# Performance work log

Measured on AMD Instinct MI355X. Metric: run time of the kernel, lower is better.

The kernel has to match this reference:

```python
import jax, jax.numpy as jnp
import numpy as np

B, T, IN, H, OUT = 512, 1024, 16, 128, 1


def _lstm_layer(x_tbd, W_ih, W_hh, b_ih, b_hh):
    """Single LSTM layer, PyTorch gate order (i, f, g, o).
    x_tbd: [T, B, D_in] -> returns [T, B, H]."""
    Tn, Bn = x_tbd.shape[0], x_tbd.shape[1]
    # Precompute input contribution for all timesteps: [T, B, 4H]
    gx = jnp.einsum('tbd,gd->tbg', x_tbd, W_ih) + b_ih + b_hh
    h0 = jnp.zeros((Bn, H), x_tbd.dtype)
    c0 = jnp.zeros((Bn, H), x_tbd.dtype)

    def step(carry, gx_t):
        h, c = carry
        gates = gx_t + h @ W_hh.T  # [B, 4H]
        i = jax.nn.sigmoid(gates[:, 0 * H:1 * H])
        f = jax.nn.sigmoid(gates[:, 1 * H:2 * H])
        g = jnp.tanh(gates[:, 2 * H:3 * H])
        o = jax.nn.sigmoid(gates[:, 3 * H:4 * H])
        c = f * c + i * g
        h = o * jnp.tanh(c)
        return (h, c), h

    _, hs = jax.lax.scan(step, (h0, c0), gx)
    return hs  # [T, B, H]


def setup_inputs() -> dict:
    key = jax.random.key(0)
    ks = jax.random.split(key, 12)
    s = 1.0 / np.sqrt(H)  # PyTorch LSTM init scale
    return {
        'x': jax.random.normal(ks[0], (B, T, IN), jnp.float32),
        'W_ih0': jax.random.uniform(ks[1], (4 * H, IN), jnp.float32, -s, s),
        'W_hh0': jax.random.uniform(ks[2], (4 * H, H), jnp.float32, -s, s),
        'b_ih0': jax.random.uniform(ks[3], (4 * H,), jnp.float32, -s, s),
        'b_hh0': jax.random.uniform(ks[4], (4 * H,), jnp.float32, -s, s),
        'W_ih1': jax.random.uniform(ks[5], (4 * H, H), jnp.float32, -s, s),
        'W_hh1': jax.random.uniform(ks[6], (4 * H, H), jnp.float32, -s, s),
        'b_ih1': jax.random.uniform(ks[7], (4 * H,), jnp.float32, -s, s),
        'b_hh1': jax.random.uniform(ks[8], (4 * H,), jnp.float32, -s, s),
        'W_fc': jax.random.uniform(ks[9], (OUT, H), jnp.float32, -s, s),
        'b_fc': jax.random.uniform(ks[10], (OUT,), jnp.float32, -s, s),
    }


def reference(x, W_ih0, W_hh0, b_ih0, b_hh0, W_ih1, W_hh1, b_ih1, b_hh1, W_fc, b_fc):
    x_tbd = jnp.transpose(x, (1, 0, 2))  # [T, B, IN]
    h1 = _lstm_layer(x_tbd, W_ih0, W_hh0, b_ih0, b_hh0)  # [T, B, H]
    h2 = _lstm_layer(h1, W_ih1, W_hh1, b_ih1, b_hh1)     # [T, B, H]
    out = jnp.transpose(h2, (1, 0, 2))  # [B, T, H]
    out = jax.nn.relu(out)
    out = out @ W_fc.T + b_fc  # [B, T, 1]
    out = jax.nn.relu(out)
    return out
```

## Files before the change

kernel.cpp:

```cpp
#include <hip/hip_runtime.h>

#define T_SEQ  1024
#define NBATCH 512
#define IN_DIM 16
#define HDIM   128
#define G4     (4 * HDIM)
#define TC     64
#define NCHUNK (T_SEQ / TC)
#define NWGH   128

typedef unsigned short ushort_t;
typedef __attribute__((ext_vector_type(8))) _Float16 f16x8;
typedef __attribute__((ext_vector_type(4))) float f32x4;

#define MFMA16(a, b, c) __builtin_amdgcn_mfma_f32_16x16x32_f16((a), (b), (c), 0, 0, 0)

__device__ __forceinline__ float sigf(float x) {
  return __builtin_amdgcn_rcpf(1.0f + __expf(-x));
}
__device__ __forceinline__ float tanhf_fast(float x) {
  return 1.0f - 2.0f * __builtin_amdgcn_rcpf(1.0f + __expf(2.0f * x));
}
__device__ __forceinline__ ushort_t f16_bits(float f) {
  const _Float16 h = (_Float16)f;
  return __builtin_bit_cast(unsigned short, h);
}
__device__ __forceinline__ void split_f16(float f, ushort_t* hi, ushort_t* lo) {
  const _Float16 h = (_Float16)f;
  *hi = __builtin_bit_cast(unsigned short, h);
  const _Float16 l = (_Float16)(f - (float)h);
  *lo = __builtin_bit_cast(unsigned short, l);
}
__device__ __forceinline__ void bar_lds() {
  asm volatile("s_waitcnt lgkmcnt(0)\n\ts_barrier" ::: "memory");
}

__global__ __launch_bounds__(256) void prep_weights(
    const float* __restrict__ Whh0, const float* __restrict__ Whh1,
    const float* __restrict__ Wih0, const float* __restrict__ Wih1,
    ushort_t* __restrict__ w0h, ushort_t* __restrict__ w0l,
    ushort_t* __restrict__ w1h, ushort_t* __restrict__ w1l,
    ushort_t* __restrict__ wxh, ushort_t* __restrict__ wxl,
    ushort_t* __restrict__ wi1h, ushort_t* __restrict__ wi1l)
{
  const int idx = blockIdx.x * 256 + threadIdx.x;
  if (idx < 512 * HDIM) {
    split_f16(Whh0[idx], &w0h[idx], &w0l[idx]);
    split_f16(Whh1[idx], &w1h[idx], &w1l[idx]);
    split_f16(Wih1[idx], &wi1h[idx], &wi1l[idx]);
  }
  if (idx < 512 * 32) {
    const int g = idx >> 5, k = idx & 31;
    const float f = (k < IN_DIM) ? Wih0[g * IN_DIM + k] : 0.0f;
    split_f16(f, &wxh[idx], &wxl[idx]);
  }
}

struct L0LDS {
  __align__(16) ushort_t hfA[4][144];
  __align__(16) ushort_t hfB[4][144];
  __align__(16) ushort_t xlds[4][TC][32];
  __align__(16) float gx0s[8 * 4 * 128 * 4];
};
struct L1LDS {
  __align__(16) ushort_t hfA[4][144];
  __align__(16) ushort_t hfB[4][144];
  __align__(16) ushort_t h2l[TC][4][136];
  __align__(16) float wfl[HDIM];
};

__global__ __launch_bounds__(512, 2) void lstm_pipe(
    const float* __restrict__ x,
    const ushort_t* __restrict__ w0h,
    const ushort_t* __restrict__ wxh, const ushort_t* __restrict__ wxl,
    const float* __restrict__ bih0, const float* __restrict__ bhh0,
    const ushort_t* __restrict__ wi1h,
    const ushort_t* __restrict__ w1h,
    const float* __restrict__ bih1, const float* __restrict__ bhh1,
    const float* __restrict__ Wfc, const float* __restrict__ bfc,
    float* __restrict__ out,
    float* __restrict__ h1s, float* __restrict__ c1s,
    float* __restrict__ h2s, float* __restrict__ c2s,
    ushort_t* __restrict__ h1buf,
    float* __restrict__ gx1buf,
    int ch)
{
  const int tid  = threadIdx.x;
  const int lane = tid & 63;
  const int wv   = tid >> 6;
  const int row  = lane & 15;
  const int kq   = lane >> 4;
  const int bq   = row >> 2;
  const int j    = wv * 16 + row;

  constexpr size_t POOL =
      sizeof(L0LDS) > sizeof(L1LDS) ? sizeof(L0LDS) : sizeof(L1LDS);
  __shared__ __align__(16) char pool[POOL];

  if (blockIdx.x < NWGH) {
    if (ch >= NCHUNK) return;
    L0LDS& S = *(L0LDS*)pool;
    const int w  = blockIdx.x;
    const int b0 = w * 4;

    f16x8 Bh[4][4], Bxh[4], Bxl[4];
#pragma unroll
    for (int i = 0; i < 4; ++i) {
      const int g = i * 128 + j;
#pragma unroll
      for (int kt = 0; kt < 4; ++kt)
        Bh[i][kt] = *(const f16x8*)&w0h[g * HDIM + kt * 32 + kq * 8];
      Bxh[i] = *(const f16x8*)&wxh[g * 32 + kq * 8];
      Bxl[i] = *(const f16x8*)&wxl[g * 32 + kq * 8];
    }

    {
      const int r = tid >> 1, half = tid & 1;
      const int b = r >> 6, ts = r & (TC - 1);
      const float* src =
          &x[((size_t)(b0 + b) * T_SEQ + ch * TC + ts) * IN_DIM + half * 8];
      const float4 v0 = *(const float4*)&src[0];
      const float4 v1 = *(const float4*)&src[4];
      ushort_t* dst = &S.xlds[b][ts][half * 8];
      dst[0] = f16_bits(v0.x); dst[1] = f16_bits(v0.y);
      dst[2] = f16_bits(v0.z); dst[3] = f16_bits(v0.w);
      dst[4] = f16_bits(v1.x); dst[5] = f16_bits(v1.y);
      dst[6] = f16_bits(v1.z); dst[7] = f16_bits(v1.w);
      *(float4*)&S.xlds[b][ts][16 + half * 8] = (float4){0.f, 0.f, 0.f, 0.f};
    }

    float bz[4];
#pragma unroll
    for (int i = 0; i < 4; ++i) bz[i] = bih0[i * 128 + j] + bhh0[i * 128 + j];
    float hc = h1s[(size_t)(b0 + kq) * HDIM + j];
    float cc = c1s[(size_t)(b0 + kq) * HDIM + j];
    S.hfA[kq][j] = f16_bits(hc);
    __syncthreads();

    ushort_t* hbp = h1buf + ((size_t)(ch & 1) * NWGH + w) * (TC * 4 * HDIM) +
                    (size_t)kq * HDIM + j;

#define L0_STEP(HIN, HOUT, TT)                                              \
  {                                                                         \
    const float4 zcu =                                                      \
        *(const float4*)&S.gx0s[((((TT) & 7) * 4 + kq) * 128 + j) * 4];     \
    f32x4 aH[4];                                                            \
    _Pragma("unroll") for (int i = 0; i < 4; ++i)                           \
        aH[i] = (f32x4){0.f, 0.f, 0.f, 0.f};                                \
    _Pragma("unroll") for (int kt = 0; kt < 4; ++kt) {                      \
      const f16x8 ah = *(const f16x8*)&S.HIN[bq][kt * 32 + kq * 8];         \
      _Pragma("unroll") for (int i = 0; i < 4; ++i)                         \
          aH[i] = MFMA16(ah, Bh[i][kt], aH[i]);                             \
    }                                                                       \
    const float ig = sigf(aH[0][0] + zcu.x);                                \
    const float fg = sigf(aH[1][0] + zcu.y);                                \
    const float gg = tanhf_fast(aH[2][0] + zcu.z);                          \
    const float og = sigf(aH[3][0] + zcu.w);                                \
    cc = fg * cc + ig * gg;                                                 \
    hc = og * tanhf_fast(cc);                                               \
    const ushort_t hbits = f16_bits(hc);                                    \
    S.HOUT[kq][j] = hbits;                                                  \
    *hbp = hbits;                                                           \
    hbp += 4 * HDIM;                                                        \
    bar_lds();                                                              \
  }

    for (int sc = 0; sc < TC / 8; ++sc) {
#pragma unroll
      for (int mt = 0; mt < 2; ++mt) {
        const f16x8 a =
            *(const f16x8*)&S.xlds[row & 3][sc * 8 + mt * 4 + (row >> 2)][kq * 8];
        f32x4 acc[4];
#pragma unroll
        for (int i = 0; i < 4; ++i) acc[i] = (f32x4){0.f, 0.f, 0.f, 0.f};
#pragma unroll
        for (int i = 0; i < 4; ++i) acc[i] = MFMA16(a, Bxh[i], acc[i]);
#pragma unroll
        for (int i = 0; i < 4; ++i) acc[i] = MFMA16(a, Bxl[i], acc[i]);
#pragma unroll
        for (int r = 0; r < 4; ++r) {
          float4 o;
          o.x = acc[0][r] + bz[0];
          o.y = acc[1][r] + bz[1];
          o.z = acc[2][r] + bz[2];
          o.w = acc[3][r] + bz[3];
          *(float4*)&S.gx0s[(((mt * 4 + kq) * 4 + r) * 128 + j) * 4] = o;
        }
      }
      bar_lds();
#pragma unroll 1
      for (int q = 0; q < 4; ++q) {
        const int tt = sc * 8 + q * 2;
        L0_STEP(hfA, hfB, tt);
        L0_STEP(hfB, hfA, tt + 1);
      }
    }
#undef L0_STEP

    h1s[(size_t)(b0 + kq) * HDIM + j] = hc;
    c1s[(size_t)(b0 + kq) * HDIM + j] = cc;
  } else {
    if (ch == 0) return;
    L1LDS& S = *(L1LDS*)pool;
    const int w  = blockIdx.x - NWGH;
    const int b0 = w * 4;

    const ushort_t* hb =
        h1buf + ((size_t)((ch - 1) & 1) * NWGH + w) * (TC * 4 * HDIM);
    float* gx = gx1buf + (size_t)w * (TC * 4 * HDIM * 4);

    if (tid < HDIM) S.wfl[tid] = Wfc[tid];

    {
      f16x8 Gh[4][4];
      float bz1[4];
#pragma unroll
      for (int i = 0; i < 4; ++i) {
        const int g = i * 128 + j;
#pragma unroll
        for (int kt = 0; kt < 4; ++kt)
          Gh[i][kt] = *(const f16x8*)&wi1h[g * HDIM + kt * 32 + kq * 8];
        bz1[i] = bih1[i * 128 + j] + bhh1[i * 128 + j];
      }
#pragma unroll 2
      for (int mt = 0; mt < TC * 4 / 16; ++mt) {
        f32x4 acc[4];
#pragma unroll
        for (int i = 0; i < 4; ++i) acc[i] = (f32x4){0.f, 0.f, 0.f, 0.f};
#pragma unroll
        for (int kt = 0; kt < 4; ++kt) {
          const f16x8 a =
              *(const f16x8*)&hb[(size_t)(mt * 16 + row) * HDIM + kt * 32 + kq * 8];
#pragma unroll
          for (int i = 0; i < 4; ++i) acc[i] = MFMA16(a, Gh[i][kt], acc[i]);
        }
#pragma unroll
        for (int r = 0; r < 4; ++r) {
          const int m = mt * 16 + kq * 4 + r;
          float4 o;
          o.x = acc[0][r] + bz1[0];
          o.y = acc[1][r] + bz1[1];
          o.z = acc[2][r] + bz1[2];
          o.w = acc[3][r] + bz1[3];
          *(float4*)&gx[((size_t)m * HDIM + j) * 4] = o;
        }
      }
    }

    float hc = h2s[(size_t)(b0 + kq) * HDIM + j];
    float cc = c2s[(size_t)(b0 + kq) * HDIM + j];
    S.hfA[kq][j] = f16_bits(hc);
    __syncthreads();

    f16x8 Rh[4][4];
#pragma unroll
    for (int i = 0; i < 4; ++i) {
      const int g = i * 128 + j;
#pragma unroll
      for (int kt = 0; kt < 4; ++kt)
        Rh[i][kt] = *(const f16x8*)&w1h[g * HDIM + kt * 32 + kq * 8];
    }

    const float4* gxp = (const float4*)&gx[((size_t)kq * HDIM + j) * 4];
    float4 zcc = *gxp;
    gxp += 512;

#define L1_STEP(HIN, HOUT, TT)                                              \
  {                                                                         \
    const float4 zcu = zcc;                                                 \
    if ((TT) + 1 < TC) { zcc = *gxp; gxp += 512; }                          \
    f32x4 aH[4];                                                            \
    _Pragma("unroll") for (int i = 0; i < 4; ++i)                           \
        aH[i] = (f32x4){0.f, 0.f, 0.f, 0.f};                                \
    _Pragma("unroll") for (int kt = 0; kt < 4; ++kt) {                      \
      const f16x8 ah = *(const f16x8*)&S.HIN[bq][kt * 32 + kq * 8];         \
      _Pragma("unroll") for (int i = 0; i < 4; ++i)                         \
          aH[i] = MFMA16(ah, Rh[i][kt], aH[i]);                             \
    }                                                                       \
    const float ig = sigf(aH[0][0] + zcu.x);                                \
    const float fg = sigf(aH[1][0] + zcu.y);                                \
    const float gg = tanhf_fast(aH[2][0] + zcu.z);                          \
    const float og = sigf(aH[3][0] + zcu.w);                                \
    cc = fg * cc + ig * gg;                                                 \
    hc = og * tanhf_fast(cc);                                               \
    const ushort_t hbits = f16_bits(hc);                                    \
    S.HOUT[kq][j] = hbits;                                                  \
    S.h2l[TT][kq][j] = hbits;                                               \
    bar_lds();                                                              \
  }

    for (int tt = 0; tt < TC; tt += 2) {
      L1_STEP(hfA, hfB, tt);
      L1_STEP(hfB, hfA, tt + 1);
    }
#undef L1_STEP

    h2s[(size_t)(b0 + kq) * HDIM + j] = hc;
    c2s[(size_t)(b0 + kq) * HDIM + j] = cc;

    if (tid < TC * 4) {
      const int tt = tid >> 2, b = tid & 3;
      const float bfcv = bfc[0];
      float s0 = 0.f, s1 = 0.f, s2 = 0.f, s3 = 0.f;
#pragma unroll
      for (int q = 0; q < HDIM / 8; ++q) {
        const f16x8 hv = *(const f16x8*)&S.h2l[tt][b][q * 8];
        const float* wq = &S.wfl[q * 8];
        s0 += fmaxf((float)hv[0], 0.f) * wq[0];
        s1 += fmaxf((float)hv[1], 0.f) * wq[1];
        s2 += fmaxf((float)hv[2], 0.f) * wq[2];
        s3 += fmaxf((float)hv[3], 0.f) * wq[3];
        s0 += fmaxf((float)hv[4], 0.f) * wq[4];
        s1 += fmaxf((float)hv[5], 0.f) * wq[5];
        s2 += fmaxf((float)hv[6], 0.f) * wq[6];
        s3 += fmaxf((float)hv[7], 0.f) * wq[7];
      }
      const float s = s0 + s1 + s2 + s3 + bfcv;
      out[(size_t)(b0 + b) * T_SEQ + (ch - 1) * TC + tt] = fmaxf(s, 0.0f);
    }
  }
}

extern "C" void kernel_launch(void* const* d_in, const int* in_sizes, int n_in,
                              void* d_out, int out_size, void* d_ws, size_t ws_size,
                              hipStream_t stream)
{
  const float* x    = (const float*)d_in[0];
  const float* Wih0 = (const float*)d_in[1];
  const float* Whh0 = (const float*)d_in[2];
  const float* bih0 = (const float*)d_in[3];
  const float* bhh0 = (const float*)d_in[4];
  const float* Wih1 = (const float*)d_in[5];
  const float* Whh1 = (const float*)d_in[6];
  const float* bih1 = (const float*)d_in[7];
  const float* bhh1 = (const float*)d_in[8];
  const float* Wfc  = (const float*)d_in[9];
  const float* bfc  = (const float*)d_in[10];
  float* out = (float*)d_out;

  const size_t stateN = (size_t)NBATCH * HDIM;
  float* h1s = (float*)d_ws;
  float* c1s = h1s + stateN;
  float* h2s = c1s + stateN;
  float* c2s = h2s + stateN;
  ushort_t* w0h  = (ushort_t*)(c2s + stateN);
  ushort_t* w0l  = w0h  + stateN;
  ushort_t* w1h  = w0l  + stateN;
  ushort_t* w1l  = w1h  + stateN;
  ushort_t* wi1h = w1l  + stateN;
  ushort_t* wi1l = wi1h + stateN;
  ushort_t* wxh  = wi1l + stateN;
  ushort_t* wxl  = wxh  + 512 * 32;
  ushort_t* h1buf = wxl + 512 * 32;
  float* gx1buf = (float*)(h1buf + (size_t)2 * NWGH * TC * 4 * HDIM);

  (void)hipMemsetAsync(d_ws, 0, 4 * stateN * sizeof(float), stream);
  hipLaunchKernelGGL(prep_weights, dim3(256), dim3(256), 0, stream,
                     Whh0, Whh1, Wih0, Wih1,
                     w0h, w0l, w1h, w1l, wxh, wxl, wi1h, wi1l);

  for (int ch = 0; ch <= NCHUNK; ++ch) {
    hipLaunchKernelGGL(lstm_pipe, dim3(2 * NWGH), dim3(512), 0, stream,
                       x, w0h, wxh, wxl, bih0, bhh0,
                       wi1h, w1h, bih1, bhh1, Wfc, bfc,
                       out, h1s, c1s, h2s, c2s, h1buf, gx1buf, ch);
  }
}
```

Baseline: 926.7 us.

## Co-schedule both LSTM layers in one 1024-thread workgroup with lockstep barriers

Instead of separate workgroups for layer 0 and layer 1, each 1024-thread block runs layer 0 in its first 512 threads and layer 1 in the second 512. Inactive halves execute matching dummy barrier loops so both halves step in lockstep. Layer 1's input projection is moved from a single upfront pass into per-8-step sub-chunks, and the input-weight fragments are reloaded inside the loop to reduce live registers. This halves the grid and co-locates the layers on one CU. In exchange, each layer now waits on the other's step latency, and the 1024-thread bound limits VGPRs per thread, which may cause spills.

```diff
diff --git a/kernel.cpp b/kernel.cpp
--- a/kernel.cpp
+++ b/kernel.cpp
@@ -69,7 +69,7 @@
   __align__(16) float wfl[HDIM];
 };
 
-__global__ __launch_bounds__(512, 2) void lstm_pipe(
+__global__ __launch_bounds__(1024) void lstm_pipe(
     const float* __restrict__ x,
     const ushort_t* __restrict__ w0h,
     const ushort_t* __restrict__ wxh, const ushort_t* __restrict__ wxl,
@@ -86,47 +86,51 @@
     int ch)
 {
   const int tid  = threadIdx.x;
+  const int ltid = tid & 511;
   const int lane = tid & 63;
-  const int wv   = tid >> 6;
+  const int wv   = (tid >> 6) & 7;
   const int row  = lane & 15;
   const int kq   = lane >> 4;
   const int bq   = row >> 2;
   const int j    = wv * 16 + row;
-
-  constexpr size_t POOL =
-      sizeof(L0LDS) > sizeof(L1LDS) ? sizeof(L0LDS) : sizeof(L1LDS);
-  __shared__ __align__(16) char pool[POOL];
-
-  if (blockIdx.x < NWGH) {
-    if (ch >= NCHUNK) return;
-    L0LDS& S = *(L0LDS*)pool;
-    const int w  = blockIdx.x;
-    const int b0 = w * 4;
-
-    f16x8 Bh[4][4], Bxh[4], Bxl[4];
+  const int w    = blockIdx.x;
+  const int b0   = w * 4;
+
+  __shared__ L0LDS S0;
+  __shared__ L1LDS S1;
+
+  if (tid < 512) {
+    if (ch >= NCHUNK) {
+      __syncthreads();
+      for (int sc = 0; sc < TC / 8; ++sc) {
+        __syncthreads();
+        for (int q = 0; q < 8; ++q) bar_lds();
+      }
+      return;
+    }
+
+    f16x8 Bh[4][4];
 #pragma unroll
     for (int i = 0; i < 4; ++i) {
       const int g = i * 128 + j;
 #pragma unroll
       for (int kt = 0; kt < 4; ++kt)
         Bh[i][kt] = *(const f16x8*)&w0h[g * HDIM + kt * 32 + kq * 8];
-      Bxh[i] = *(const f16x8*)&wxh[g * 32 + kq * 8];
-      Bxl[i] = *(const f16x8*)&wxl[g * 32 + kq * 8];
     }
 
     {
-      const int r = tid >> 1, half = tid & 1;
+      const int r = ltid >> 1, half = ltid & 1;
       const int b = r >> 6, ts = r & (TC - 1);
       const float* src =
           &x[((size_t)(b0 + b) * T_SEQ + ch * TC + ts) * IN_DIM + half * 8];
       const float4 v0 = *(const float4*)&src[0];
       const float4 v1 = *(const float4*)&src[4];
-      ushort_t* dst = &S.xlds[b][ts][half * 8];
+      ushort_t* dst = &S0.xlds[b][ts][half * 8];
       dst[0] = f16_bits(v0.x); dst[1] = f16_bits(v0.y);
       dst[2] = f16_bits(v0.z); dst[3] = f16_bits(v0.w);
       dst[4] = f16_bits(v1.x); dst[5] = f16_bits(v1.y);
       dst[6] = f16_bits(v1.z); dst[7] = f16_bits(v1.w);
-      *(float4*)&S.xlds[b][ts][16 + half * 8] = (float4){0.f, 0.f, 0.f, 0.f};
+      *(float4*)&S0.xlds[b][ts][16 + half * 8] = (float4){0.f, 0.f, 0.f, 0.f};
     }
 
     float bz[4];
@@ -134,7 +138,7 @@
     for (int i = 0; i < 4; ++i) bz[i] = bih0[i * 128 + j] + bhh0[i * 128 + j];
     float hc = h1s[(size_t)(b0 + kq) * HDIM + j];
     float cc = c1s[(size_t)(b0 + kq) * HDIM + j];
-    S.hfA[kq][j] = f16_bits(hc);
+    S0.hfA[kq][j] = f16_bits(hc);
     __syncthreads();
 
     ushort_t* hbp = h1buf + ((size_t)(ch & 1) * NWGH + w) * (TC * 4 * HDIM) +
@@ -143,12 +147,12 @@
 #define L0_STEP(HIN, HOUT, TT)                                              \
   {                                                                         \
     const float4 zcu =                                                      \
-        *(const float4*)&S.gx0s[((((TT) & 7) * 4 + kq) * 128 + j) * 4];     \
+        *(const float4*)&S0.gx0s[((((TT) & 7) * 4 + kq) * 128 + j) * 4];    \
     f32x4 aH[4];                                                            \
     _Pragma("unroll") for (int i = 0; i < 4; ++i)                           \
         aH[i] = (f32x4){0.f, 0.f, 0.f, 0.f};                                \
     _Pragma("unroll") for (int kt = 0; kt < 4; ++kt) {                      \
-      const f16x8 ah = *(const f16x8*)&S.HIN[bq][kt * 32 + kq * 8];         \
+      const f16x8 ah = *(const f16x8*)&S0.HIN[bq][kt * 32 + kq * 8];        \
       _Pragma("unroll") for (int i = 0; i < 4; ++i)                         \
           aH[i] = MFMA16(ah, Bh[i][kt], aH[i]);                             \
     }                                                                       \
@@ -159,35 +163,44 @@
     cc = fg * cc + ig * gg;                                                 \
     hc = og * tanhf_fast(cc);                                               \
     const ushort_t hbits = f16_bits(hc);                                    \
-    S.HOUT[kq][j] = hbits;                                                  \
+    S0.HOUT[kq][j] = hbits;                                                 \
     *hbp = hbits;                                                           \
     hbp += 4 * HDIM;                                                        \
     bar_lds();                                                              \
   }
 
     for (int sc = 0; sc < TC / 8; ++sc) {
-#pragma unroll
-      for (int mt = 0; mt < 2; ++mt) {
-        const f16x8 a =
-            *(const f16x8*)&S.xlds[row & 3][sc * 8 + mt * 4 + (row >> 2)][kq * 8];
-        f32x4 acc[4];
-#pragma unroll
-        for (int i = 0; i < 4; ++i) acc[i] = (f32x4){0.f, 0.f, 0.f, 0.f};
-#pragma unroll
-        for (int i = 0; i < 4; ++i) acc[i] = MFMA16(a, Bxh[i], acc[i]);
-#pragma unroll
-        for (int i = 0; i < 4; ++i) acc[i] = MFMA16(a, Bxl[i], acc[i]);
-#pragma unroll
-        for (int r = 0; r < 4; ++r) {
-          float4 o;
-          o.x = acc[0][r] + bz[0];
-          o.y = acc[1][r] + bz[1];
-          o.z = acc[2][r] + bz[2];
-          o.w = acc[3][r] + bz[3];
-          *(float4*)&S.gx0s[(((mt * 4 + kq) * 4 + r) * 128 + j) * 4] = o;
+      {
+        f16x8 Bxh[4], Bxl[4];
+#pragma unroll
+        for (int i = 0; i < 4; ++i) {
+          const int g = i * 128 + j;
+          Bxh[i] = *(const f16x8*)&wxh[g * 32 + kq * 8];
+          Bxl[i] = *(const f16x8*)&wxl[g * 32 + kq * 8];
         }
-      }
-      bar_lds();
+#pragma unroll
+        for (int mt = 0; mt < 2; ++mt) {
+          const f16x8 a = *(const f16x8*)
+              &S0.xlds[row & 3][sc * 8 + mt * 4 + (row >> 2)][kq * 8];
+          f32x4 acc[4];
+#pragma unroll
+          for (int i = 0; i < 4; ++i) acc[i] = (f32x4){0.f, 0.f, 0.f, 0.f};
+#pragma unroll
+          for (int i = 0; i < 4; ++i) acc[i] = MFMA16(a, Bxh[i], acc[i]);
+#pragma unroll
+          for (int i = 0; i < 4; ++i) acc[i] = MFMA16(a, Bxl[i], acc[i]);
+#pragma unroll
+          for (int r = 0; r < 4; ++r) {
+            float4 o;
+            o.x = acc[0][r] + bz[0];
+            o.y = acc[1][r] + bz[1];
+            o.z = acc[2][r] + bz[2];
+            o.w = acc[3][r] + bz[3];
+            *(float4*)&S0.gx0s[(((mt * 4 + kq) * 4 + r) * 128 + j) * 4] = o;
+          }
+        }
+      }
+      __syncthreads();
 #pragma unroll 1
       for (int q = 0; q < 4; ++q) {
         const int tt = sc * 8 + q * 2;
@@ -200,112 +213,125 @@
     h1s[(size_t)(b0 + kq) * HDIM + j] = hc;
     c1s[(size_t)(b0 + kq) * HDIM + j] = cc;
   } else {
-    if (ch == 0) return;
-    L1LDS& S = *(L1LDS*)pool;
-    const int w  = blockIdx.x - NWGH;
-    const int b0 = w * 4;
+    if (ch == 0) {
+      __syncthreads();
+      for (int sc = 0; sc < TC / 8; ++sc) {
+        __syncthreads();
+        for (int q = 0; q < 8; ++q) bar_lds();
+      }
+      return;
+    }
 
     const ushort_t* hb =
         h1buf + ((size_t)((ch - 1) & 1) * NWGH + w) * (TC * 4 * HDIM);
     float* gx = gx1buf + (size_t)w * (TC * 4 * HDIM * 4);
 
-    if (tid < HDIM) S.wfl[tid] = Wfc[tid];
-
-    {
-      f16x8 Gh[4][4];
-      float bz1[4];
-#pragma unroll
-      for (int i = 0; i < 4; ++i) {
-        const int g = i * 128 + j;
-#pragma unroll
-        for (int kt = 0; kt < 4; ++kt)
-          Gh[i][kt] = *(const f16x8*)&wi1h[g * HDIM + kt * 32 + kq * 8];
-        bz1[i] = bih1[i * 128 + j] + bhh1[i * 128 + j];
-      }
-#pragma unroll 2
-      for (int mt = 0; mt < TC * 4 / 16; ++mt) {
-        f32x4 acc[4];
-#pragma unroll
-        for (int i = 0; i < 4; ++i) acc[i] = (f32x4){0.f, 0.f, 0.f, 0.f};
-#pragma unroll
-        for (int kt = 0; kt < 4; ++kt) {
-          const f16x8 a =
-              *(const f16x8*)&hb[(size_t)(mt * 16 + row) * HDIM + kt * 32 + kq * 8];
-#pragma unroll
-          for (int i = 0; i < 4; ++i) acc[i] = MFMA16(a, Gh[i][kt], acc[i]);
-        }
-#pragma unroll
-        for (int r = 0; r < 4; ++r) {
-          const int m = mt * 16 + kq * 4 + r;
-          float4 o;
-          o.x = acc[0][r] + bz1[0];
-          o.y = acc[1][r] + bz1[1];
-          o.z = acc[2][r] + bz1[2];
-          o.w = acc[3][r] + bz1[3];
-          *(float4*)&gx[((size_t)m * HDIM + j) * 4] = o;
-        }
-      }
+    if (ltid < HDIM) S1.wfl[ltid] = Wfc[ltid];
+
+    float bz1[4];
+#pragma unroll
+    for (int i = 0; i < 4; ++i) bz1[i] = bih1[i * 128 + j] + bhh1[i * 128 + j];
+    f16x8 Rh[4][4];
+#pragma unroll
+    for (int i = 0; i < 4; ++i) {
+      const int g = i * 128 + j;
+#pragma unroll
+      for (int kt = 0; kt < 4; ++kt)
+        Rh[i][kt] = *(const f16x8*)&w1h[g * HDIM + kt * 32 + kq * 8];
     }
 
     float hc = h2s[(size_t)(b0 + kq) * HDIM + j];
     float cc = c2s[(size_t)(b0 + kq) * HDIM + j];
-    S.hfA[kq][j] = f16_bits(hc);
+    S1.hfA[kq][j] = f16_bits(hc);
     __syncthreads();
 
-    f16x8 Rh[4][4];
-#pragma unroll
-    for (int i = 0; i < 4; ++i) {
-      const int g = i * 128 + j;
-#pragma unroll
-      for (int kt = 0; kt < 4; ++kt)
-        Rh[i][kt] = *(const f16x8*)&w1h[g * HDIM + kt * 32 + kq * 8];
-    }
-
-    const float4* gxp = (const float4*)&gx[((size_t)kq * HDIM + j) * 4];
-    float4 zcc = *gxp;
-    gxp += 512;
-
-#define L1_STEP(HIN, HOUT, TT)                                              \
+#define L1_STEP(HIN, HOUT, TT, ZCU)                                         \
   {                                                                         \
-    const float4 zcu = zcc;                                                 \
-    if ((TT) + 1 < TC) { zcc = *gxp; gxp += 512; }                          \
     f32x4 aH[4];                                                            \
     _Pragma("unroll") for (int i = 0; i < 4; ++i)                           \
         aH[i] = (f32x4){0.f, 0.f, 0.f, 0.f};                                \
     _Pragma("unroll") for (int kt = 0; kt < 4; ++kt) {                      \
-      const f16x8 ah = *(const f16x8*)&S.HIN[bq][kt * 32 + kq * 8];         \
+      const f16x8 ah = *(const f16x8*)&S1.HIN[bq][kt * 32 + kq * 8];        \
       _Pragma("unroll") for (int i = 0; i < 4; ++i)                         \
           aH[i] = MFMA16(ah, Rh[i][kt], aH[i]);                             \
     }                                                                       \
-    const float ig = sigf(aH[0][0] + zcu.x);                                \
-    const float fg = sigf(aH[1][0] + zcu.y);                                \
-    const float gg = tanhf_fast(aH[2][0] + zcu.z);                          \
-    const float og = sigf(aH[3][0] + zcu.w);                                \
+    const float ig = sigf(aH[0][0] + (ZCU).x);                              \
+    const float fg = sigf(aH[1][0] + (ZCU).y);                              \
+    const float gg = tanhf_fast(aH[2][0] + (ZCU).z);                        \
+    const float og = sigf(aH[3][0] + (ZCU).w);                              \
     cc = fg * cc + ig * gg;                                                 \
     hc = og * tanhf_fast(cc);                                               \
     const ushort_t hbits = f16_bits(hc);                                    \
-    S.HOUT[kq][j] = hbits;                                                  \
-    S.h2l[TT][kq][j] = hbits;                                               \
+    S1.HOUT[kq][j] = hbits;                                                 \
+    S1.h2l[TT][kq][j] = hbits;                                              \
     bar_lds();                                                              \
   }
 
-    for (int tt = 0; tt < TC; tt += 2) {
-      L1_STEP(hfA, hfB, tt);
-      L1_STEP(hfB, hfA, tt + 1);
+    for (int sc = 0; sc < TC / 8; ++sc) {
+      {
+        f16x8 Gh[4][4];
+#pragma unroll
+        for (int i = 0; i < 4; ++i) {
+          const int g = i * 128 + j;
+#pragma unroll
+          for (int kt = 0; kt < 4; ++kt)
+            Gh[i][kt] = *(const f16x8*)&wi1h[g * HDIM + kt * 32 + kq * 8];
+        }
+#pragma unroll
+        for (int mt2 = 0; mt2 < 2; ++mt2) {
+          const int m0 = sc * 32 + mt2 * 16;
+          f32x4 acc[4];
+#pragma unroll
+          for (int i = 0; i < 4; ++i) acc[i] = (f32x4){0.f, 0.f, 0.f, 0.f};
+#pragma unroll
+          for (int kt = 0; kt < 4; ++kt) {
+            const f16x8 a =
+                *(const f16x8*)&hb[(size_t)(m0 + row) * HDIM + kt * 32 + kq * 8];
+#pragma unroll
+            for (int i = 0; i < 4; ++i) acc[i] = MFMA16(a, Gh[i][kt], acc[i]);
+          }
+#pragma unroll
+          for (int r = 0; r < 4; ++r) {
+            const int m = m0 + kq * 4 + r;
+            float4 o;
+            o.x = acc[0][r] + bz1[0];
+            o.y = acc[1][r] + bz1[1];
+            o.z = acc[2][r] + bz1[2];
+            o.w = acc[3][r] + bz1[3];
+            *(float4*)&gx[((size_t)m * HDIM + j) * 4] = o;
+          }
+        }
+      }
+      __syncthreads();
+
+      const float4* gxp =
+          (const float4*)gx + ((size_t)(sc * 8 * 4 + kq) * HDIM + j);
+      float4 zcc = *gxp;
+      gxp += 512;
+#pragma unroll 1
+      for (int q = 0; q < 4; ++q) {
+        const int tt = sc * 8 + q * 2;
+        float4 z0 = zcc;
+        zcc = *gxp; gxp += 512;
+        L1_STEP(hfA, hfB, tt, z0);
+        float4 z1 = zcc;
+        if (q < 3) { zcc = *gxp; gxp += 512; }
+        L1_STEP(hfB, hfA, tt + 1, z1);
+      }
     }
 #undef L1_STEP
 
     h2s[(size_t)(b0 + kq) * HDIM + j] = hc;
     c2s[(size_t)(b0 + kq) * HDIM + j] = cc;
 
-    if (tid < TC * 4) {
-      const int tt = tid >> 2, b = tid & 3;
+    if (ltid < TC * 4) {
+      const int tt = ltid >> 2, b = ltid & 3;
       const float bfcv = bfc[0];
       float s0 = 0.f, s1 = 0.f, s2 = 0.f, s3 = 0.f;
 #pragma unroll
       for (int q = 0; q < HDIM / 8; ++q) {
-        const f16x8 hv = *(const f16x8*)&S.h2l[tt][b][q * 8];
-        const float* wq = &S.wfl[q * 8];
+        const f16x8 hv = *(const f16x8*)&S1.h2l[tt][b][q * 8];
+        const float* wq = &S1.wfl[q * 8];
         s0 += fmaxf((float)hv[0], 0.f) * wq[0];
         s1 += fmaxf((float)hv[1], 0.f) * wq[1];
         s2 += fmaxf((float)hv[2], 0.f) * wq[2];
@@ -360,7 +386,7 @@
                      w0h, w0l, w1h, w1l, wxh, wxl, wi1h, wi1l);
 
   for (int ch = 0; ch <= NCHUNK; ++ch) {
-    hipLaunchKernelGGL(lstm_pipe, dim3(2 * NWGH), dim3(512), 0, stream,
+    hipLaunchKernelGGL(lstm_pipe, dim3(NWGH), dim3(1024), 0, stream,
                        x, w0h, wxh, wxl, bih0, bhh0,
                        wi1h, w1h, bih1, bhh1, Wfc, bfc,
                        out, h1s, c1s, h2s, c2s, h1buf, gx1buf, ch);
```

New measurement: 2.273 ms. 145% more time.

## Process eight batch rows per workgroup and interleave layer-1 input projection per subchunk

Applied to the files above, without the earlier changes.

Halves the number of workgroups per layer and gives each one 8 batch rows, so every recurrent step issues two independent MFMA chains that share the same register-resident weights. This is meant to hide the latency of the serial recurrence chain. Layer 1 now computes its input-gate projection in 4-step subchunks interleaved with the recurrence rather than all upfront, keeps both weight sets resident in registers, and writes h2 to a global buffer instead of LDS for the final FC. The trade-off is more register pressure, fewer active CUs, and an extra global round trip for the FC stage.

```diff
diff --git a/kernel.cpp b/kernel.cpp
--- a/kernel.cpp
+++ b/kernel.cpp
@@ -7,7 +7,7 @@
 #define G4     (4 * HDIM)
 #define TC     64
 #define NCHUNK (T_SEQ / TC)
-#define NWGH   128
+#define NWGH   64
 
 typedef unsigned short ushort_t;
 typedef __attribute__((ext_vector_type(8))) _Float16 f16x8;
@@ -57,15 +57,14 @@
 }
 
 struct L0LDS {
-  __align__(16) ushort_t hfA[4][144];
-  __align__(16) ushort_t hfB[4][144];
-  __align__(16) ushort_t xlds[4][TC][32];
-  __align__(16) float gx0s[8 * 4 * 128 * 4];
+  __align__(16) ushort_t hfA[8][144];
+  __align__(16) ushort_t hfB[8][144];
+  __align__(16) ushort_t xlds[8][TC][32];
+  __align__(16) float gx0s[4 * 8 * 128 * 4];
 };
 struct L1LDS {
-  __align__(16) ushort_t hfA[4][144];
-  __align__(16) ushort_t hfB[4][144];
-  __align__(16) ushort_t h2l[TC][4][136];
+  __align__(16) ushort_t hfA[8][144];
+  __align__(16) ushort_t hfB[8][144];
   __align__(16) float wfl[HDIM];
 };
 
@@ -82,6 +81,7 @@
     float* __restrict__ h1s, float* __restrict__ c1s,
     float* __restrict__ h2s, float* __restrict__ c2s,
     ushort_t* __restrict__ h1buf,
+    ushort_t* __restrict__ h2buf,
     float* __restrict__ gx1buf,
     int ch)
 {
@@ -93,15 +93,13 @@
   const int bq   = row >> 2;
   const int j    = wv * 16 + row;
 
-  constexpr size_t POOL =
-      sizeof(L0LDS) > sizeof(L1LDS) ? sizeof(L0LDS) : sizeof(L1LDS);
-  __shared__ __align__(16) char pool[POOL];
+  __shared__ L0LDS S0;
+  __shared__ L1LDS S1;
 
   if (blockIdx.x < NWGH) {
     if (ch >= NCHUNK) return;
-    L0LDS& S = *(L0LDS*)pool;
     const int w  = blockIdx.x;
-    const int b0 = w * 4;
+    const int b0 = w * 8;
 
     f16x8 Bh[4][4], Bxh[4], Bxl[4];
 #pragma unroll
@@ -114,62 +112,88 @@
       Bxl[i] = *(const f16x8*)&wxl[g * 32 + kq * 8];
     }
 
-    {
-      const int r = tid >> 1, half = tid & 1;
-      const int b = r >> 6, ts = r & (TC - 1);
+#pragma unroll
+    for (int q = 0; q < 2; ++q) {
+      const int idx  = q * 512 + tid;
+      const int half = idx & 1;
+      const int ts   = (idx >> 1) & (TC - 1);
+      const int b    = idx >> 7;
       const float* src =
           &x[((size_t)(b0 + b) * T_SEQ + ch * TC + ts) * IN_DIM + half * 8];
       const float4 v0 = *(const float4*)&src[0];
       const float4 v1 = *(const float4*)&src[4];
-      ushort_t* dst = &S.xlds[b][ts][half * 8];
+      ushort_t* dst = &S0.xlds[b][ts][half * 8];
       dst[0] = f16_bits(v0.x); dst[1] = f16_bits(v0.y);
       dst[2] = f16_bits(v0.z); dst[3] = f16_bits(v0.w);
       dst[4] = f16_bits(v1.x); dst[5] = f16_bits(v1.y);
       dst[6] = f16_bits(v1.z); dst[7] = f16_bits(v1.w);
-      *(float4*)&S.xlds[b][ts][16 + half * 8] = (float4){0.f, 0.f, 0.f, 0.f};
+      *(float4*)&S0.xlds[b][ts][16 + half * 8] = (float4){0.f, 0.f, 0.f, 0.f};
     }
 
     float bz[4];
 #pragma unroll
     for (int i = 0; i < 4; ++i) bz[i] = bih0[i * 128 + j] + bhh0[i * 128 + j];
-    float hc = h1s[(size_t)(b0 + kq) * HDIM + j];
-    float cc = c1s[(size_t)(b0 + kq) * HDIM + j];
-    S.hfA[kq][j] = f16_bits(hc);
+    float hc0 = h1s[(size_t)(b0 + kq) * HDIM + j];
+    float cc0 = c1s[(size_t)(b0 + kq) * HDIM + j];
+    float hc1 = h1s[(size_t)(b0 + 4 + kq) * HDIM + j];
+    float cc1 = c1s[(size_t)(b0 + 4 + kq) * HDIM + j];
+    S0.hfA[kq][j]     = f16_bits(hc0);
+    S0.hfA[4 + kq][j] = f16_bits(hc1);
     __syncthreads();
 
-    ushort_t* hbp = h1buf + ((size_t)(ch & 1) * NWGH + w) * (TC * 4 * HDIM) +
+    ushort_t* hbp = h1buf + ((size_t)(ch & 1) * NWGH + w) * (TC * 8 * HDIM) +
                     (size_t)kq * HDIM + j;
 
 #define L0_STEP(HIN, HOUT, TT)                                              \
   {                                                                         \
-    const float4 zcu =                                                      \
-        *(const float4*)&S.gx0s[((((TT) & 7) * 4 + kq) * 128 + j) * 4];     \
-    f32x4 aH[4];                                                            \
-    _Pragma("unroll") for (int i = 0; i < 4; ++i)                           \
-        aH[i] = (f32x4){0.f, 0.f, 0.f, 0.f};                                \
+    const float4 z0 =                                                       \
+        *(const float4*)&S0.gx0s[((((TT) & 3) * 8 + kq) * 128 + j) * 4];    \
+    const float4 z1 =                                                       \
+        *(const float4*)&S0.gx0s[((((TT) & 3) * 8 + 4 + kq) * 128 + j) * 4];\
+    f32x4 a0[4], a1[4];                                                     \
+    _Pragma("unroll") for (int i = 0; i < 4; ++i) {                         \
+      a0[i] = (f32x4){0.f, 0.f, 0.f, 0.f};                                  \
+      a1[i] = (f32x4){0.f, 0.f, 0.f, 0.f};                                  \
+    }                                                                       \
     _Pragma("unroll") for (int kt = 0; kt < 4; ++kt) {                      \
-      const f16x8 ah = *(const f16x8*)&S.HIN[bq][kt * 32 + kq * 8];         \
+      const f16x8 ah0 = *(const f16x8*)&S0.HIN[bq][kt * 32 + kq * 8];       \
+      const f16x8 ah1 = *(const f16x8*)&S0.HIN[4 + bq][kt * 32 + kq * 8];   \
       _Pragma("unroll") for (int i = 0; i < 4; ++i)                         \
-          aH[i] = MFMA16(ah, Bh[i][kt], aH[i]);                             \
-    }                                                                       \
-    const float ig = sigf(aH[0][0] + zcu.x);                                \
-    const float fg = sigf(aH[1][0] + zcu.y);                                \
-    const float gg = tanhf_fast(aH[2][0] + zcu.z);                          \
-    const float og = sigf(aH[3][0] + zcu.w);                                \
-    cc = fg * cc + ig * gg;                                                 \
-    hc = og * tanhf_fast(cc);                                               \
-    const ushort_t hbits = f16_bits(hc);                                    \
-    S.HOUT[kq][j] = hbits;                                                  \
-    *hbp = hbits;                                                           \
-    hbp += 4 * HDIM;                                                        \
+          a0[i] = MFMA16(ah0, Bh[i][kt], a0[i]);                            \
+      _Pragma("unroll") for (int i = 0; i < 4; ++i)                         \
+          a1[i] = MFMA16(ah1, Bh[i][kt], a1[i]);                            \
+    }                                                                       \
+    {                                                                       \
+      const float ig = sigf(a0[0][0] + z0.x);                               \
+      const float fg = sigf(a0[1][0] + z0.y);                               \
+      const float gg = tanhf_fast(a0[2][0] + z0.z);                         \
+      const float og = sigf(a0[3][0] + z0.w);                               \
+      cc0 = fg * cc0 + ig * gg;                                             \
+      hc0 = og * tanhf_fast(cc0);                                           \
+      const ushort_t hb0 = f16_bits(hc0);                                   \
+      S0.HOUT[kq][j] = hb0;                                                 \
+      hbp[0] = hb0;                                                         \
+    }                                                                       \
+    {                                                                       \
+      const float ig = sigf(a1[0][0] + z1.x);                               \
+      const float fg = sigf(a1[1][0] + z1.y);                               \
+      const float gg = tanhf_fast(a1[2][0] + z1.z);                         \
+      const float og = sigf(a1[3][0] + z1.w);                               \
+      cc1 = fg * cc1 + ig * gg;                                             \
+      hc1 = og * tanhf_fast(cc1);                                           \
+      const ushort_t hb1 = f16_bits(hc1);                                   \
+      S0.HOUT[4 + kq][j] = hb1;                                             \
+      hbp[4 * HDIM] = hb1;                                                  \
+    }                                                                       \
+    hbp += 8 * HDIM;                                                        \
     bar_lds();                                                              \
   }
 
-    for (int sc = 0; sc < TC / 8; ++sc) {
-#pragma unroll
-      for (int mt = 0; mt < 2; ++mt) {
-        const f16x8 a =
-            *(const f16x8*)&S.xlds[row & 3][sc * 8 + mt * 4 + (row >> 2)][kq * 8];
+    for (int sc = 0; sc < TC / 4; ++sc) {
+#pragma unroll
+      for (int g = 0; g < 2; ++g) {
+        const f16x8 a = *(const f16x8*)
+            &S0.xlds[g * 4 + (row & 3)][sc * 4 + (row >> 2)][kq * 8];
         f32x4 acc[4];
 #pragma unroll
         for (int i = 0; i < 4; ++i) acc[i] = (f32x4){0.f, 0.f, 0.f, 0.f};
@@ -184,128 +208,169 @@
           o.y = acc[1][r] + bz[1];
           o.z = acc[2][r] + bz[2];
           o.w = acc[3][r] + bz[3];
-          *(float4*)&S.gx0s[(((mt * 4 + kq) * 4 + r) * 128 + j) * 4] = o;
+          *(float4*)&S0.gx0s[((kq * 8 + g * 4 + r) * 128 + j) * 4] = o;
         }
       }
       bar_lds();
-#pragma unroll 1
-      for (int q = 0; q < 4; ++q) {
-        const int tt = sc * 8 + q * 2;
-        L0_STEP(hfA, hfB, tt);
-        L0_STEP(hfB, hfA, tt + 1);
-      }
+      const int t0s = sc * 4;
+      L0_STEP(hfA, hfB, t0s);
+      L0_STEP(hfB, hfA, t0s + 1);
+      L0_STEP(hfA, hfB, t0s + 2);
+      L0_STEP(hfB, hfA, t0s + 3);
     }
 #undef L0_STEP
 
-    h1s[(size_t)(b0 + kq) * HDIM + j] = hc;
-    c1s[(size_t)(b0 + kq) * HDIM + j] = cc;
+    h1s[(size_t)(b0 + kq) * HDIM + j]     = hc0;
+    c1s[(size_t)(b0 + kq) * HDIM + j]     = cc0;
+    h1s[(size_t)(b0 + 4 + kq) * HDIM + j] = hc1;
+    c1s[(size_t)(b0 + 4 + kq) * HDIM + j] = cc1;
   } else {
     if (ch == 0) return;
-    L1LDS& S = *(L1LDS*)pool;
     const int w  = blockIdx.x - NWGH;
-    const int b0 = w * 4;
+    const int b0 = w * 8;
 
     const ushort_t* hb =
-        h1buf + ((size_t)((ch - 1) & 1) * NWGH + w) * (TC * 4 * HDIM);
-    float* gx = gx1buf + (size_t)w * (TC * 4 * HDIM * 4);
-
-    if (tid < HDIM) S.wfl[tid] = Wfc[tid];
-
-    {
-      f16x8 Gh[4][4];
-      float bz1[4];
-#pragma unroll
-      for (int i = 0; i < 4; ++i) {
-        const int g = i * 128 + j;
-#pragma unroll
-        for (int kt = 0; kt < 4; ++kt)
-          Gh[i][kt] = *(const f16x8*)&wi1h[g * HDIM + kt * 32 + kq * 8];
-        bz1[i] = bih1[i * 128 + j] + bhh1[i * 128 + j];
-      }
-#pragma unroll 2
-      for (int mt = 0; mt < TC * 4 / 16; ++mt) {
+        h1buf + ((size_t)((ch - 1) & 1) * NWGH + w) * (TC * 8 * HDIM);
+    float* gx = gx1buf + (size_t)w * (TC * 8 * HDIM * 4);
+    ushort_t* h2p = h2buf + (size_t)w * (TC * 8 * HDIM) +
+                    (size_t)kq * HDIM + j;
+
+    if (tid < HDIM) S1.wfl[tid] = Wfc[tid];
+
+    float bz1[4];
+#pragma unroll
+    for (int i = 0; i < 4; ++i) bz1[i] = bih1[i * 128 + j] + bhh1[i * 128 + j];
+    f16x8 Rh[4][4], Gh[4][4];
+#pragma unroll
+    for (int i = 0; i < 4; ++i) {
+      const int g = i * 128 + j;
+#pragma unroll
+      for (int kt = 0; kt < 4; ++kt) {
+        Rh[i][kt] = *(const f16x8*)&w1h[g * HDIM + kt * 32 + kq * 8];
+        Gh[i][kt] = *(const f16x8*)&wi1h[g * HDIM + kt * 32 + kq * 8];
+      }
+    }
+
+    float hc0 = h2s[(size_t)(b0 + kq) * HDIM + j];
+    float cc0 = c2s[(size_t)(b0 + kq) * HDIM + j];
+    float hc1 = h2s[(size_t)(b0 + 4 + kq) * HDIM + j];
+    float cc1 = c2s[(size_t)(b0 + 4 + kq) * HDIM + j];
+    S1.hfA[kq][j]     = f16_bits(hc0);
+    S1.hfA[4 + kq][j] = f16_bits(hc1);
+    __syncthreads();
+
+#define L1_STEP(HIN, HOUT, TT, Z0, Z1)                                      \
+  {                                                                         \
+    f32x4 a0[4], a1[4];                                                     \
+    _Pragma("unroll") for (int i = 0; i < 4; ++i) {                         \
+      a0[i] = (f32x4){0.f, 0.f, 0.f, 0.f};                                  \
+      a1[i] = (f32x4){0.f, 0.f, 0.f, 0.f};                                  \
+    }                                                                       \
+    _Pragma("unroll") for (int kt = 0; kt < 4; ++kt) {                      \
+      const f16x8 ah0 = *(const f16x8*)&S1.HIN[bq][kt * 32 + kq * 8];       \
+      const f16x8 ah1 = *(const f16x8*)&S1.HIN[4 + bq][kt * 32 + kq * 8];   \
+      _Pragma("unroll") for (int i = 0; i < 4; ++i)                         \
+          a0[i] = MFMA16(ah0, Rh[i][kt], a0[i]);                            \
+      _Pragma("unroll") for (int i = 0; i < 4; ++i)                         \
+          a1[i] = MFMA16(ah1, Rh[i][kt], a1[i]);                            \
+    }                                                                       \
+    {                                                                       \
+      const float ig = sigf(a0[0][0] + (Z0).x);                             \
+      const float fg = sigf(a0[1][0] + (Z0).y);                             \
+      const float gg = tanhf_fast(a0[2][0] + (Z0).z);                       \
+      const float og = sigf(a0[3][0] + (Z0).w);                             \
+      cc0 = fg * cc0 + ig * gg;                                             \
+      hc0 = og * tanhf_fast(cc0);                                           \
+      const ushort_t hb0 = f16_bits(hc0);                                   \
+      S1.HOUT[kq][j] = hb0;                                                 \
+      h2p[0] = hb0;                                                         \
+    }                                                                       \
+    {                                                                       \
+      const float ig = sigf(a1[0][0] + (Z1).x);                             \
+      const float fg = sigf(a1[1][0] + (Z1).y);                             \
+      const float gg = tanhf_fast(a1[2][0] + (Z1).z);                       \
+      const float og = sigf(a1[3][0] + (Z1).w);                             \
+      cc1 = fg * cc1 + ig * gg;                                             \
+      hc1 = og * tanhf_fast(cc1);                                           \
+      const ushort_t hb1 = f16_bits(hc1);                                   \
+      S1.HOUT[4 + kq][j] = hb1;                                             \
+      h2p[4 * HDIM] = hb1;                                                  \
+    }                                                                       \
+    h2p += 8 * HDIM;                                                        \
+    bar_lds();                                                              \
+  }
+
+    for (int sc = 0; sc < TC / 4; ++sc) {
+#pragma unroll
+      for (int g = 0; g < 2; ++g) {
+        const f16x8 a = *(const f16x8*)&hb[
+            (size_t)((sc * 4 + (row >> 2)) * 8 + g * 4 + (row & 3)) * HDIM +
+            0 * 32 + kq * 8];
         f32x4 acc[4];
 #pragma unroll
         for (int i = 0; i < 4; ++i) acc[i] = (f32x4){0.f, 0.f, 0.f, 0.f};
 #pragma unroll
         for (int kt = 0; kt < 4; ++kt) {
-          const f16x8 a =
-              *(const f16x8*)&hb[(size_t)(mt * 16 + row) * HDIM + kt * 32 + kq * 8];
-#pragma unroll
-          for (int i = 0; i < 4; ++i) acc[i] = MFMA16(a, Gh[i][kt], acc[i]);
+          const f16x8 av = *(const f16x8*)&hb[
+              (size_t)((sc * 4 + (row >> 2)) * 8 + g * 4 + (row & 3)) * HDIM +
+              kt * 32 + kq * 8];
+#pragma unroll
+          for (int i = 0; i < 4; ++i) acc[i] = MFMA16(av, Gh[i][kt], acc[i]);
         }
+        (void)a;
 #pragma unroll
         for (int r = 0; r < 4; ++r) {
-          const int m = mt * 16 + kq * 4 + r;
+          const int m = (sc * 4 + kq) * 8 + g * 4 + r;
           float4 o;
           o.x = acc[0][r] + bz1[0];
           o.y = acc[1][r] + bz1[1];
           o.z = acc[2][r] + bz1[2];
           o.w = acc[3][r] + bz1[3];
-          *(float4*)&gx[((size_t)m * HDIM + j) * 4] = o;
+          *(float4*)&gx[((size_t)m * 128 + j) * 4] = o;
         }
       }
-    }
-
-    float hc = h2s[(size_t)(b0 + kq) * HDIM + j];
-    float cc = c2s[(size_t)(b0 + kq) * HDIM + j];
-    S.hfA[kq][j] = f16_bits(hc);
+      __syncthreads();
+
+      const float4* zp =
+          (const float4*)gx + ((size_t)(sc * 4) * 8 + kq) * 128 + j;
+      float4 zc0 = zp[0], zc1 = zp[512];
+      zp += 1024;
+      const int t0s = sc * 4;
+      {
+        float4 u0 = zc0, u1 = zc1;
+        zc0 = zp[0]; zc1 = zp[512]; zp += 1024;
+        L1_STEP(hfA, hfB, t0s, u0, u1);
+      }
+      {
+        float4 u0 = zc0, u1 = zc1;
+        zc0 = zp[0]; zc1 = zp[512]; zp += 1024;
+        L1_STEP(hfB, hfA, t0s + 1, u0, u1);
+      }
+      {
+        float4 u0 = zc0, u1 = zc1;
+        zc0 = zp[0]; zc1 = zp[512];
+        L1_STEP(hfA, hfB, t0s + 2, u0, u1);
+      }
+      L1_STEP(hfB, hfA, t0s + 3, zc0, zc1);
+    }
+#undef L1_STEP
+
+    h2s[(size_t)(b0 + kq) * HDIM + j]     = hc0;
+    c2s[(size_t)(b0 + kq) * HDIM + j]     = cc0;
+    h2s[(size_t)(b0 + 4 + kq) * HDIM + j] = hc1;
+    c2s[(size_t)(b0 + 4 + kq) * HDIM + j] = cc1;
     __syncthreads();
 
-    f16x8 Rh[4][4];
-#pragma unroll
-    for (int i = 0; i < 4; ++i) {
-      const int g = i * 128 + j;
-#pragma unroll
-      for (int kt = 0; kt < 4; ++kt)
-        Rh[i][kt] = *(const f16x8*)&w1h[g * HDIM + kt * 32 + kq * 8];
-    }
-
-    const float4* gxp = (const float4*)&gx[((size_t)kq * HDIM + j) * 4];
-    float4 zcc = *gxp;
-    gxp += 512;
-
-#define L1_STEP(HIN, HOUT, TT)                                              \
-  {                                                                         \
-    const float4 zcu = zcc;                                                 \
-    if ((TT) + 1 < TC) { zcc = *gxp; gxp += 512; }                          \
-    f32x4 aH[4];                                                            \
-    _Pragma("unroll") for (int i = 0; i < 4; ++i)                           \
-        aH[i] = (f32x4){0.f, 0.f, 0.f, 0.f};                                \
-    _Pragma("unroll") for (int kt = 0; kt < 4; ++kt) {                      \
-      const f16x8 ah = *(const f16x8*)&S.HIN[bq][kt * 32 + kq * 8];         \
-      _Pragma("unroll") for (int i = 0; i < 4; ++i)                         \
-          aH[i] = MFMA16(ah, Rh[i][kt], aH[i]);                             \
-    }                                                                       \
-    const float ig = sigf(aH[0][0] + zcu.x);                                \
-    const float fg = sigf(aH[1][0] + zcu.y);                                \
-    const float gg = tanhf_fast(aH[2][0] + zcu.z);                          \
-    const float og = sigf(aH[3][0] + zcu.w);                                \
-    cc = fg * cc + ig * gg;                                                 \
-    hc = og * tanhf_fast(cc);                                               \
-    const ushort_t hbits = f16_bits(hc);                                    \
-    S.HOUT[kq][j] = hbits;                                                  \
-    S.h2l[TT][kq][j] = hbits;                                               \
-    bar_lds();                                                              \
-  }
-
-    for (int tt = 0; tt < TC; tt += 2) {
-      L1_STEP(hfA, hfB, tt);
-      L1_STEP(hfB, hfA, tt + 1);
-    }
-#undef L1_STEP
-
-    h2s[(size_t)(b0 + kq) * HDIM + j] = hc;
-    c2s[(size_t)(b0 + kq) * HDIM + j] = cc;
-
-    if (tid < TC * 4) {
-      const int tt = tid >> 2, b = tid & 3;
+    {
+      const int tt = tid >> 3, b = tid & 7;
+      const ushort_t* hrow =
+          h2buf + (size_t)w * (TC * 8 * HDIM) + (size_t)tid * HDIM;
       const float bfcv = bfc[0];
       float s0 = 0.f, s1 = 0.f, s2 = 0.f, s3 = 0.f;
 #pragma unroll
       for (int q = 0; q < HDIM / 8; ++q) {
-        const f16x8 hv = *(const f16x8*)&S.h2l[tt][b][q * 8];
-        const float* wq = &S.wfl[q * 8];
+        const f16x8 hv = *(const f16x8*)&hrow[q * 8];
+        const float* wq = &S1.wfl[q * 8];
         s0 += fmaxf((float)hv[0], 0.f) * wq[0];
         s1 += fmaxf((float)hv[1], 0.f) * wq[1];
         s2 += fmaxf((float)hv[2], 0.f) * wq[2];
@@ -352,7 +417,8 @@
   ushort_t* wxh  = wi1l + stateN;
   ushort_t* wxl  = wxh  + 512 * 32;
   ushort_t* h1buf = wxl + 512 * 32;
-  float* gx1buf = (float*)(h1buf + (size_t)2 * NWGH * TC * 4 * HDIM);
+  ushort_t* h2buf = h1buf + (size_t)2 * NWGH * TC * 8 * HDIM;
+  float* gx1buf = (float*)(h2buf + (size_t)NWGH * TC * 8 * HDIM);
 
   (void)hipMemsetAsync(d_ws, 0, 4 * stateN * sizeof(float), stream);
   hipLaunchKernelGGL(prep_weights, dim3(256), dim3(256), 0, stream,
@@ -363,6 +429,6 @@
     hipLaunchKernelGGL(lstm_pipe, dim3(2 * NWGH), dim3(512), 0, stream,
                        x, w0h, wxh, wxl, bih0, bhh0,
                        wi1h, w1h, bih1, bhh1, Wfc, bfc,
-                       out, h1s, c1s, h2s, c2s, h1buf, gx1buf, ch);
-  }
-}
+                       out, h1s, c1s, h2s, c2s, h1buf, h2buf, gx1buf, ch);
+  }
+}
```

Measured after the change: 1.807 ms. +94.9%, slower.
